# Kernel optimization log

Hardware: AMD Instinct MI355X
Metric: run time of the kernel (lower is better)

Reference implementation:

```python
import jax, jax.numpy as jnp
import numpy as np

WS = 8   # window_size
SS = 4   # shift_size = window_size // 2
HEADS = 8
DH = 16  # dim_head


def _rel_index(ws):
    c = np.arange(ws)
    coords = np.stack(np.meshgrid(c, c, indexing='ij')).reshape(2, -1)  # [2, ws*ws]
    rel = (coords[:, :, None] - coords[:, None, :]).transpose(1, 2, 0)  # [l, l, 2]
    rel[..., 0] += ws - 1
    rel[..., 1] += ws - 1
    rel[..., 0] *= 2 * ws - 1
    return rel.sum(-1)  # [l, l] int


def _make_mask(H, W, ws, ss):
    img = np.zeros((H, W), np.float32)
    sl = (slice(0, -ws), slice(-ws, -ss), slice(-ss, None))
    cnt = 0
    for hs in sl:
        for wcs in sl:
            img[hs, wcs] = cnt
            cnt += 1
    win = img.reshape(H // ws, ws, W // ws, ws).transpose(0, 2, 1, 3).reshape(-1, ws * ws)
    diff = win[:, None, :] - win[:, :, None]  # [nW, l, l]
    return np.where(diff != 0, -np.inf, 0.0).astype(np.float32)


def _ln(x, g, b, eps=1e-5):
    m = x.mean(-1, keepdims=True)
    v = ((x - m) ** 2).mean(-1, keepdims=True)
    return (x - m) * jax.lax.rsqrt(v + eps) * g + b


def _part(t, ws):
    B, H, W, C = t.shape
    return t.reshape(B, H // ws, ws, W // ws, ws, C).transpose(0, 1, 3, 2, 4, 5).reshape(-1, ws * ws, C)


def _unpart(t, ws, B, H, W):
    C = t.shape[-1]
    return t.reshape(B, H // ws, W // ws, ws, ws, C).transpose(0, 1, 3, 2, 4, 5).reshape(B, H, W, C)


def _block(x, illu, p, shift, mask, ridx):
    B, H, W, C = x.shape
    ws = WS
    l = ws * ws
    g1, b1, qw, qb, tbl, pw, pb, g2, b2, f1w, f1b, f2w, f2b = p
    shortcut = x
    xn = _ln(x, g1, b1)
    if shift > 0:
        xn = jnp.roll(xn, (-shift, -shift), (1, 2))
        illu = jnp.roll(illu, (-shift, -shift), (1, 2))
    xw = _part(xn, ws)     # [n, l, C]
    iw = _part(illu, ws)   # [n, l, C]
    n = xw.shape[0]
    qkv = (xw @ qw + qb).reshape(n, l, 3, HEADS, DH).transpose(2, 0, 3, 1, 4)
    q, k, v = qkv[0], qkv[1], qkv[2]  # each [n, h, l, d]
    attn = jnp.einsum('nhld,nhmd->nhlm', q * (DH ** -0.5), k)
    bias = tbl[ridx].transpose(2, 0, 1)  # [h, l, l]
    attn = attn + bias[None]
    # illumination modulation of V
    v = v * iw.reshape(n, l, HEADS, DH).transpose(0, 2, 1, 3)
    if mask is not None:
        nw = mask.shape[0]
        attn = (attn.reshape(B, nw, HEADS, l, l) + mask[None, :, None]).reshape(n, HEADS, l, l)
    attn = jax.nn.softmax(attn, axis=-1)
    out = jnp.einsum('nhlm,nhmd->nhld', attn, v).transpose(0, 2, 1, 3).reshape(n, l, C)
    out = out @ pw + pb
    out = _unpart(out, ws, B, H, W)
    if shift > 0:
        out = jnp.roll(out, (shift, shift), (1, 2))
    x = shortcut + out
    y = _ln(x, g2, b2)
    y = jax.nn.gelu(y @ f1w + f1b, approximate=False) @ f2w + f2b
    return x + y


def setup_inputs() -> dict:
    key = jax.random.key(0)
    ks = jax.random.split(key, 8)
    B, C, H, W = 4, 128, 256, 256
    NB, HID, TBL = 2, 512, 225
    r = lambda k, s, sc=1.0: jax.random.normal(k, s, jnp.float32) * sc
    return {
        'x': r(ks[0], (B, C, H, W)),
        'illu_fea': r(ks[1], (B, C, H, W)),
        'norm1_g': jnp.ones((NB, C), jnp.float32),
        'norm1_b': jnp.zeros((NB, C), jnp.float32),
        'qkv_w': r(ks[2], (NB, C, 3 * C), 0.02),
        'qkv_b': jnp.zeros((NB, 3 * C), jnp.float32),
        'bias_table': r(ks[3], (NB, TBL, HEADS), 0.02),
        'proj_w': r(ks[4], (NB, C, C), 0.02),
        'proj_b': jnp.zeros((NB, C), jnp.float32),
        'norm2_g': jnp.ones((NB, C), jnp.float32),
        'norm2_b': jnp.zeros((NB, C), jnp.float32),
        'fc1_w': r(ks[5], (NB, C, HID), 0.02),
        'fc1_b': jnp.zeros((NB, HID), jnp.float32),
        'fc2_w': r(ks[6], (NB, HID, C), 0.02),
        'fc2_b': jnp.zeros((NB, C), jnp.float32),
    }


def reference(x, illu_fea, norm1_g, norm1_b, qkv_w, qkv_b, bias_table, proj_w, proj_b, norm2_g, norm2_b, fc1_w, fc1_b, fc2_w, fc2_b):
    B, C, H, W = x.shape
    xb = x.transpose(0, 2, 3, 1)
    ib = illu_fea.transpose(0, 2, 3, 1)
    ridx = _rel_index(WS)
    mask = jnp.asarray(_make_mask(H, W, WS, SS))
    nb = norm1_g.shape[0]
    for i in range(nb):
        shift = 0 if i % 2 == 0 else SS
        p = (norm1_g[i], norm1_b[i], qkv_w[i], qkv_b[i], bias_table[i], proj_w[i], proj_b[i],
             norm2_g[i], norm2_b[i], fc1_w[i], fc1_b[i], fc2_w[i], fc2_b[i])
        xb = _block(xb, ib, p, shift, mask if shift > 0 else None, ridx)
    return xb.transpose(0, 3, 1, 2)
```

## Files before the change

### kernel.cpp

```cpp
#include <hip/hip_runtime.h>
#include <hip/hip_bf16.h>

typedef unsigned short u16;
typedef __attribute__((ext_vector_type(8))) short bfrag;
typedef __attribute__((ext_vector_type(4))) float f32x4;
typedef __attribute__((ext_vector_type(2))) int i32x2;
typedef __attribute__((ext_vector_type(4))) int i32x4;

constexpr int OFF_N1G  = 64;
constexpr int OFF_N1B  = OFF_N1G + 256;
constexpr int OFF_QKVB = OFF_N1B + 256;
constexpr int OFF_PB   = OFF_QKVB + 768;
constexpr int OFF_N2G  = OFF_PB + 256;
constexpr int OFF_N2B  = OFF_N2G + 256;
constexpr int OFF_F1B  = OFF_N2B + 256;
constexpr int OFF_F2B  = OFF_F1B + 1024;
constexpr int OFF_BIAS = OFF_F2B + 256;
constexpr int OFF_QWT  = OFF_BIAS + 65536;
constexpr int OFF_PWT  = OFF_QWT + 49152;
constexpr int OFF_F1WT = OFF_PWT + 16384;
constexpr int OFF_F2WT = OFF_F1WT + 65536;
constexpr long OFF_OBUF = 265728;
constexpr long OFF_XBUF = OFF_OBUF + 16777216;
constexpr long OFF_IBUF = OFF_XBUF + 33554432;

__device__ __forceinline__ float blo(unsigned w) { return __uint_as_float(w << 16); }
__device__ __forceinline__ u16 f2b(float f) {
  unsigned u = __float_as_uint(f);
  u += 0x7fffu + ((u >> 16) & 1u);
  return (u16)(u >> 16);
}
__device__ __forceinline__ unsigned f2b_pk(float a, float b) {
  unsigned r;
  asm("v_cvt_pk_bf16_f32 %0, %1, %2" : "=v"(r) : "v"(a), "v"(b));
  return r;
}
__device__ __forceinline__ float ldin(const void* p, long i, int bf) {
  if (bf) return blo((unsigned)((const u16*)p)[i]);
  return ((const float*)p)[i];
}
__device__ __forceinline__ f32x4 mfma16(bfrag a, bfrag b, f32x4 c) {
  return __builtin_amdgcn_mfma_f32_16x16x32_bf16(a, b, c, 0, 0, 0);
}
__device__ __forceinline__ float fast_gelu(float x) {
  const float z = fabsf(x) * 0.70710678118f;
  const float tt = __builtin_amdgcn_rcpf(1.0f + 0.3275911f * z);
  const float poly = tt * (0.254829592f + tt * (-0.284496736f + tt * (1.421413741f +
                     tt * (-1.453152027f + tt * 1.061405429f))));
  const float erfz = 1.0f - poly * __expf(-z * z);
  return x * 0.5f * (1.0f + copysignf(erfz, x));
}

__global__ void k_sniff(const u16* __restrict__ x, int* __restrict__ flag) {
  __shared__ int sc[4];
  const int t = threadIdx.x;
  int c = 0;
  for (int i = t; i < 4096; i += 256) {
    const int e = (x[2 * i] >> 7) & 0xFF;
    c += (e >= 96 && e <= 143) ? 1 : 0;
  }
  #pragma unroll
  for (int o = 32; o; o >>= 1) c += __shfl_down(c, o);
  if ((t & 63) == 0) sc[t >> 6] = c;
  __syncthreads();
  if (t == 0) *flag = ((sc[0] + sc[1] + sc[2] + sc[3]) > 2400) ? 1 : 0;
}

__global__ void k_convert(const void* __restrict__ src, float* __restrict__ dst, int n,
                          const int* __restrict__ flagp) {
  const int bf = *flagp;
  const int i = blockIdx.x * 256 + threadIdx.x;
  if (i < n) dst[i] = ldin(src, i, bf);
}

__global__ void k_cvtT(const void* __restrict__ src, u16* __restrict__ dst, int K, int N,
                       const int* __restrict__ flagp) {
  const int bf = *flagp;
  const int id = blockIdx.x * 256 + threadIdx.x;
  const int KN = K * N;
  if (id >= 2 * KN) return;
  const int l = id / KN, r = id % KN;
  const int n = r % N, k = r / N;
  const float v = ldin(src, (long)l * KN + (long)k * N + n, bf);
  dst[((long)l * N + n) * K + k] = f2b(v);
}

__global__ void k_cvtF1(const void* __restrict__ src, u16* __restrict__ dst,
                        const int* __restrict__ flagp) {
  const int bf = *flagp;
  const int id = blockIdx.x * 256 + threadIdx.x;
  const int l = id >> 16, r = id & 65535;
  const int k = r >> 9, n = r & 511;
  const float v = ldin(src, (long)l * 65536 + k * 512 + n, bf);
  dst[(long)l * 65536 + (n >> 6) * 8192 + (((n & 63) * 128 + k) ^ ((n & 7) << 3))] = f2b(v);
}
__global__ void k_cvtF2(const void* __restrict__ src, u16* __restrict__ dst,
                        const int* __restrict__ flagp) {
  const int bf = *flagp;
  const int id = blockIdx.x * 256 + threadIdx.x;
  const int l = id >> 16, r = id & 65535;
  const int k = r >> 7, n = r & 127;
  const float v = ldin(src, (long)l * 65536 + k * 128 + n, bf);
  dst[(long)l * 65536 + (k >> 6) * 8192 + ((n * 64 + (k & 63)) ^ ((n & 7) << 3))] = f2b(v);
}

__global__ void k_bias(const void* __restrict__ tbl, float* __restrict__ dst,
                       const int* __restrict__ flagp) {
  const int bf = *flagp;
  const int id = blockIdx.x * 256 + threadIdx.x;
  const int j = id & 63, i = (id >> 6) & 63;
  const int idx = ((i >> 3) - (j >> 3) + 7) * 15 + ((i & 7) - (j & 7) + 7);
  const int h = (id >> 12) & 7, l = id >> 15;
  dst[(id & ~4095) + j * 64 + i] = ldin(tbl, (long)l * 1800 + idx * 8 + h, bf);
}

__global__ __launch_bounds__(256) void k_tin(const void* __restrict__ src,
                                             const void* __restrict__ il,
                                             float* __restrict__ dst,
                                             u16* __restrict__ idst,
                                             const int* __restrict__ flagp) {
  __shared__ float tile[64][65];
  const int bf = *flagp;
  const int bid = blockIdx.x;
  const int cb = bid & 1, wb = (bid >> 1) & 3, h = (bid >> 3) & 255, b = bid >> 11;
  const int tw = threadIdx.x & 63, tg = threadIdx.x >> 6;
  #pragma unroll
  for (int i = 0; i < 16; ++i) {
    const int c = i * 4 + tg;
    tile[c][tw] = ldin(src, ((long)((b * 128 + cb * 64 + c) * 256 + h)) * 256 + wb * 64 + tw, bf);
  }
  __syncthreads();
  #pragma unroll
  for (int i = 0; i < 16; ++i) {
    const int wl = i * 4 + tg;
    const int pix = (b * 256 + h) * 256 + wb * 64 + wl;
    dst[(size_t)pix * 128 + cb * 64 + tw] = tile[tw][wl];
  }
  __syncthreads();
  #pragma unroll
  for (int i = 0; i < 16; ++i) {
    const int c = i * 4 + tg;
    tile[c][tw] = ldin(il, ((long)((b * 128 + cb * 64 + c) * 256 + h)) * 256 + wb * 64 + tw, bf);
  }
  __syncthreads();
  #pragma unroll
  for (int i = 0; i < 16; ++i) {
    const int wl = i * 4 + tg;
    const int pix = (b * 256 + h) * 256 + wb * 64 + wl;
    idst[(size_t)pix * 128 + cb * 64 + tw] = f2b(tile[tw][wl]);
  }
}

__device__ __forceinline__ int xn_addr(int tok, int chunk) {
  return tok * 128 + ((chunk ^ (tok & 7)) << 3);
}

__global__ __launch_bounds__(256, 5) void k_attnB(
    const float* __restrict__ xbuf, const u16* __restrict__ ibuf,
    const float* __restrict__ wsf, u16* __restrict__ obuf,
    const u16* __restrict__ qwT, const float* __restrict__ biasb,
    const int blk, const int shift)
{
  __shared__ __align__(16) u16 smem[12288];
  u16* xn = smem;
  u16* Q2 = smem;
  u16* K2 = smem + 4096;
  u16* VT = smem + 8192;

  const int t = threadIdx.x, l = t & 63, w = t >> 6;
  const int bid = blockIdx.x;
  const int win = bid >> 1, hh0 = (bid & 1) * 4;
  const int b = win >> 10, wh = (win >> 5) & 31, wn = win & 31;
  const int hglob = hh0 + w;
  const int g = l >> 4, c16 = l & 15, c8 = c16 * 8;

  const float* g1 = wsf + OFF_N1G + blk * 128;
  const float* b1 = wsf + OFF_N1B + blk * 128;
  const float* qb = wsf + OFF_QKVB + blk * 384;
  const u16* qwl = qwT + (size_t)blk * 49152;

  float iw[4][4];
  {
    const u16* ip = ibuf + (size_t)b * 8388608 + hglob * 16 + c16;
    #pragma unroll
    for (int rt = 0; rt < 4; ++rt)
      #pragma unroll
      for (int r = 0; r < 4; ++r) {
        const int tok = rt * 16 + g * 4 + r;
        const int hh = (wh * 8 + (tok >> 3) + shift) & 255;
        const int wp = (wn * 8 + (tok & 7) + shift) & 255;
        iw[rt][r] = blo(ip[(size_t)((hh << 8) + wp) * 128]);
      }
  }

  {
    float gg[8], bb[8];
    *(float4*)&gg[0] = *(const float4*)(g1 + c8);
    *(float4*)&gg[4] = *(const float4*)(g1 + c8 + 4);
    *(float4*)&bb[0] = *(const float4*)(b1 + c8);
    *(float4*)&bb[4] = *(const float4*)(b1 + c8 + 4);
    #pragma unroll
    for (int s = 0; s < 4; ++s) {
      const int tok = w * 16 + s * 4 + g;
      const int hh = (wh * 8 + (tok >> 3) + shift) & 255;
      const int wp = (wn * 8 + (tok & 7) + shift) & 255;
      const float* xr = xbuf + (size_t)((b * 256 + hh) * 256 + wp) * 128 + c8;
      float v[8];
      *(float4*)&v[0] = *(const float4*)xr;
      *(float4*)&v[4] = *(const float4*)(xr + 4);
      float sm = 0.f, sq = 0.f;
      #pragma unroll
      for (int j = 0; j < 8; ++j) { sm += v[j]; sq = fmaf(v[j], v[j], sq); }
      #pragma unroll
      for (int o = 8; o; o >>= 1) { sm += __shfl_xor(sm, o); sq += __shfl_xor(sq, o); }
      const float mean = sm * 0.0078125f;
      const float rstd = rsqrtf(fmaf(-mean, mean, sq * 0.0078125f) + 1e-5f);
      unsigned pk[4];
      #pragma unroll
      for (int jj = 0; jj < 4; ++jj) {
        const float o0 = (v[2 * jj] - mean) * rstd * gg[2 * jj] + bb[2 * jj];
        const float o1 = (v[2 * jj + 1] - mean) * rstd * gg[2 * jj + 1] + bb[2 * jj + 1];
        pk[jj] = f2b_pk(o0, o1);
      }
      i32x4 st; st[0] = (int)pk[0]; st[1] = (int)pk[1]; st[2] = (int)pk[2]; st[3] = (int)pk[3];
      *(i32x4*)&xn[(tok * 128 + c8) ^ ((tok & 7) << 3)] = st;
    }
  }
  __syncthreads();

  {
    const int colv = (16 + hglob) * 16 + c16;
    const float bv = qb[colv];
    f32x4 acv[4];
    #pragma unroll
    for (int rt = 0; rt < 4; ++rt) acv[rt] = (f32x4){bv, bv, bv, bv};
    const u16* bp = qwl + colv * 128 + g * 8;
    #pragma unroll
    for (int kt = 0; kt < 4; ++kt) {
      const bfrag bw = *(const bfrag*)(bp + kt * 32);
      #pragma unroll
      for (int rt = 0; rt < 4; ++rt) {
        const bfrag a = *(const bfrag*)&xn[xn_addr(rt * 16 + c16, kt * 4 + g)];
        acv[rt] = mfma16(a, bw, acv[rt]);
      }
    }
    u16* vt = VT + w * 1024 + c16 * 64;
    const int sx = (c16 & 7) << 3;
    #pragma unroll
    for (int rt = 0; rt < 4; ++rt) {
      const unsigned p0 = f2b_pk(acv[rt][0] * iw[rt][0], acv[rt][1] * iw[rt][1]);
      const unsigned p1 = f2b_pk(acv[rt][2] * iw[rt][2], acv[rt][3] * iw[rt][3]);
      i32x2 pp; pp[0] = (int)p0; pp[1] = (int)p1;
      *(i32x2*)&vt[(rt * 16 + g * 4) ^ sx] = pp;
    }
  }

  f32x4 acq[4], ack[4];
  {
    const int colq = hglob * 16 + c16, colk = colq + 128;
    const float bq = qb[colq], bk = qb[colk];
    #pragma unroll
    for (int rt = 0; rt < 4; ++rt) {
      acq[rt] = (f32x4){bq, bq, bq, bq};
      ack[rt] = (f32x4){bk, bk, bk, bk};
    }
    const u16* bpq = qwl + colq * 128 + g * 8;
    const u16* bpk = qwl + colk * 128 + g * 8;
    #pragma unroll
    for (int kt = 0; kt < 4; ++kt) {
      const bfrag bwq = *(const bfrag*)(bpq + kt * 32);
      const bfrag bwk = *(const bfrag*)(bpk + kt * 32);
      #pragma unroll
      for (int rt = 0; rt < 4; ++rt) {
        const bfrag a = *(const bfrag*)&xn[xn_addr(rt * 16 + c16, kt * 4 + g)];
        acq[rt] = mfma16(a, bwq, acq[rt]);
        ack[rt] = mfma16(a, bwk, ack[rt]);
      }
    }
  }
  __syncthreads();

  {
    u16* dq = Q2 + w * 1024 + ((c16 >> 3) * 64) * 8 + (c16 & 7);
    u16* dk = K2 + w * 1024 + ((c16 >> 3) * 64) * 8 + (c16 & 7);
    #pragma unroll
    for (int rt = 0; rt < 4; ++rt)
      #pragma unroll
      for (int r = 0; r < 4; ++r) {
        const int tok = rt * 16 + g * 4 + r;
        dq[tok * 8] = f2b(acq[rt][r]);
        dk[tok * 8] = f2b(ack[rt][r]);
      }
  }

  const bfrag zfrag = {0, 0, 0, 0, 0, 0, 0, 0};
  const f32x4 zacc = {0.f, 0.f, 0.f, 0.f};
  bfrag kf[4];
  #pragma unroll
  for (int jt = 0; jt < 4; ++jt) {
    bfrag v = zfrag;
    if (l < 32) v = *(const bfrag*)&K2[w * 1024 + (g * 64 + jt * 16 + c16) * 8];
    kf[jt] = v;
  }
  bfrag vb[2];
  {
    const int sx = (c16 & 7) << 3;
    #pragma unroll
    for (int kt = 0; kt < 2; ++kt)
      vb[kt] = *(const bfrag*)&VT[w * 1024 + c16 * 64 + ((kt * 32 + g * 8) ^ sx)];
  }

  const float* bl2 = biasb + blk * 32768 + hglob * 4096;
  const bool mk = (shift > 0) && ((wh == 31) || (wn == 31));
  int lj[4];
  if (mk) {
    #pragma unroll
    for (int jt = 0; jt < 4; ++jt) {
      const int j = jt * 16 + c16;
      lj[jt] = ((wh == 31) ? (((j >> 3) < 4) ? 1 : 2) : 0) * 3 +
               ((wn == 31) ? (((j & 7) < 4) ? 1 : 2) : 0);
    }
  }

  u16* Pw = K2 + w * 1024;
  u16* ob = obuf + (size_t)win * 8192 + hglob * 16 + c16;

  #pragma unroll
  for (int it = 0; it < 4; ++it) {
    bfrag qf = zfrag;
    if (l < 32) qf = *(const bfrag*)&Q2[w * 1024 + (g * 64 + it * 16 + c16) * 8];
    f32x4 s4[4];
    #pragma unroll
    for (int jt = 0; jt < 4; ++jt) s4[jt] = mfma16(qf, kf[jt], zacc);

    #pragma unroll
    for (int jt = 0; jt < 4; ++jt) {
      const float4 bv4 = *(const float4*)&bl2[(jt * 16 + c16) * 64 + it * 16 + g * 4];
      #pragma unroll
      for (int r = 0; r < 4; ++r)
        s4[jt][r] = fmaf(s4[jt][r], 0.25f, (&bv4.x)[r]);
    }
    if (mk) {
      #pragma unroll
      for (int r = 0; r < 4; ++r) {
        const int i = it * 16 + g * 4 + r;
        const int li = ((wh == 31) ? (((i >> 3) < 4) ? 1 : 2) : 0) * 3 +
                       ((wn == 31) ? (((i & 7) < 4) ? 1 : 2) : 0);
        #pragma unroll
        for (int jt = 0; jt < 4; ++jt)
          if (li != lj[jt]) s4[jt][r] = -1e30f;
      }
    }

    #pragma unroll
    for (int r = 0; r < 4; ++r) {
      float mx = fmaxf(fmaxf(s4[0][r], s4[1][r]), fmaxf(s4[2][r], s4[3][r]));
      #pragma unroll
      for (int o = 8; o; o >>= 1) mx = fmaxf(mx, __shfl_xor(mx, o));
      float e0 = __expf(s4[0][r] - mx);
      float e1 = __expf(s4[1][r] - mx);
      float e2 = __expf(s4[2][r] - mx);
      float e3 = __expf(s4[3][r] - mx);
      float sm = e0 + e1 + e2 + e3;
      #pragma unroll
      for (int o = 8; o; o >>= 1) sm += __shfl_xor(sm, o);
      const float inv = 1.0f / sm;
      s4[0][r] = e0 * inv; s4[1][r] = e1 * inv;
      s4[2][r] = e2 * inv; s4[3][r] = e3 * inv;
    }

    #pragma unroll
    for (int jt = 0; jt < 4; ++jt)
      #pragma unroll
      for (int r = 0; r < 4; ++r)
        Pw[(g * 4 + r) * 40 + jt * 16 + c16] = f2b(s4[jt][r]);
    const bfrag pa0 = *(const bfrag*)&Pw[c16 * 40 + g * 8];
    const bfrag pa1 = *(const bfrag*)&Pw[c16 * 40 + 32 + g * 8];
    f32x4 o = zacc;
    o = mfma16(pa0, vb[0], o);
    o = mfma16(pa1, vb[1], o);
    #pragma unroll
    for (int r = 0; r < 4; ++r)
      ob[(it * 16 + g * 4 + r) * 128] = f2b(o[r]);
  }
}

__global__ __launch_bounds__(256) void k_proj(
    float* xbuf, const u16* __restrict__ obuf, const u16* __restrict__ pwT,
    const float* __restrict__ wsf, const int blk, const int shift)
{
  __shared__ __align__(16) u16 osh[64 * 136];
  const int t = threadIdx.x, l = t & 63, w = t >> 6;
  const int win = blockIdx.x;
  const int b = win >> 10, wh = (win >> 5) & 31, wn = win & 31;
  const u16* ob = obuf + (size_t)win * 8192;
  #pragma unroll
  for (int q = 0; q < 4; ++q) {
    const int idx = (q * 256 + t) * 8;
    *(bfrag*)&osh[(idx >> 7) * 136 + (idx & 127)] = *(const bfrag*)&ob[idx];
  }
  __syncthreads();
  bfrag af[4];
  #pragma unroll
  for (int kt = 0; kt < 4; ++kt)
    af[kt] = *(const bfrag*)&osh[(w * 16 + (l & 15)) * 136 + kt * 32 + (l >> 4) * 8];
  const u16* pwl = pwT + blk * 16384;
  const float* pb = wsf + OFF_PB + blk * 128;
  #pragma unroll
  for (int ct = 0; ct < 8; ++ct) {
    const int col = ct * 16 + (l & 15);
    const float bv = pb[col];
    f32x4 ac = {bv, bv, bv, bv};
    const u16* bp = pwl + col * 128 + (l >> 4) * 8;
    #pragma unroll
    for (int kt = 0; kt < 4; ++kt) ac = mfma16(af[kt], *(const bfrag*)(bp + kt * 32), ac);
    #pragma unroll
    for (int r = 0; r < 4; ++r) {
      const int tok = w * 16 + (l >> 4) * 4 + r;
      const int hh = (wh * 8 + (tok >> 3) + shift) & 255;
      const int wp = (wn * 8 + (tok & 7) + shift) & 255;
      const size_t xi = (size_t)((b * 256 + hh) * 256 + wp) * 128 + col;
      xbuf[xi] += ac[r];
    }
  }
}

__global__ __launch_bounds__(256, 3) void k_ffn(
    float* xbuf, const float* __restrict__ wsf,
    const u16* __restrict__ f1S, const u16* __restrict__ f2S,
    const int blk, void* __restrict__ outp, const int last,
    const int* __restrict__ flagp)
{
  __shared__ __align__(16) u16 B0[8192];
  __shared__ __align__(16) u16 B1[8192];
  __shared__ __align__(16) u16 hid[8192];
  __shared__ float sbias[512];
  const int bfl = *flagp;
  const int t = threadIdx.x, l = t & 63, w = t >> 6;
  u16* hw = hid + w * 2048;
  const int pix0 = blockIdx.x * 64;
  const float* g2 = wsf + OFF_N2G + blk * 128;
  const float* b2 = wsf + OFF_N2B + blk * 128;
  const float* f1bp = wsf + OFF_F1B + blk * 512;
  const float* f2bp = wsf + OFF_F2B + blk * 128;
  const u16* f1 = f1S + (size_t)blk * 65536;
  const u16* f2 = f2S + (size_t)blk * 65536;

  auto STAGE = [&](const u16* src, u16* dstbuf) {
    const u16* gp = src + w * 2048 + l * 8;
    u16* d = dstbuf + w * 2048;
    #pragma unroll
    for (int q = 0; q < 4; ++q)
      __builtin_amdgcn_global_load_lds(gp + q * 512, d + q * 512, 16, 0, 0);
  };
  auto tsrc = [&](int i) -> const u16* {
    const int cc = i >> 2, pp = i & 3;
    return (pp < 2 ? f1 : f2) + cc * 16384 + (pp & 1) * 8192;
  };

  STAGE(tsrc(0), B0);
  sbias[t] = f1bp[t];
  sbias[t + 256] = f1bp[t + 256];

  {
    const int g = l >> 4, c16 = l & 15, c8 = c16 * 8;
    float gg[8], bb[8];
    *(float4*)&gg[0] = *(const float4*)(g2 + c8);
    *(float4*)&gg[4] = *(const float4*)(g2 + c8 + 4);
    *(float4*)&bb[0] = *(const float4*)(b2 + c8);
    *(float4*)&bb[4] = *(const float4*)(b2 + c8 + 4);
    #pragma unroll
    for (int s = 0; s < 4; ++s) {
      const int tt = s * 4 + g;
      const float* xr = xbuf + (size_t)(pix0 + w * 16 + tt) * 128 + c8;
      float v[8];
      *(float4*)&v[0] = *(const float4*)xr;
      *(float4*)&v[4] = *(const float4*)(xr + 4);
      float sm = 0.f, sq = 0.f;
      #pragma unroll
      for (int j = 0; j < 8; ++j) { sm += v[j]; sq = fmaf(v[j], v[j], sq); }
      #pragma unroll
      for (int o = 8; o; o >>= 1) { sm += __shfl_xor(sm, o); sq += __shfl_xor(sq, o); }
      const float mean = sm * 0.0078125f;
      const float rstd = rsqrtf(fmaf(-mean, mean, sq * 0.0078125f) + 1e-5f);
      unsigned pk[4];
      #pragma unroll
      for (int jj = 0; jj < 4; ++jj) {
        const float o0 = (v[2 * jj] - mean) * rstd * gg[2 * jj] + bb[2 * jj];
        const float o1 = (v[2 * jj + 1] - mean) * rstd * gg[2 * jj + 1] + bb[2 * jj + 1];
        pk[jj] = f2b_pk(o0, o1);
      }
      i32x4 st; st[0] = (int)pk[0]; st[1] = (int)pk[1]; st[2] = (int)pk[2]; st[3] = (int)pk[3];
      *(i32x4*)&hw[(tt * 128 + c8) ^ ((tt & 7) << 3)] = st;
    }
  }
  bfrag af[4];
  #pragma unroll
  for (int kt = 0; kt < 4; ++kt)
    af[kt] = *(const bfrag*)&hw[((l & 15) * 128 + kt * 32 + (l >> 4) * 8) ^ (((l & 15) & 7) << 3)];

  f32x4 y[8];
  #pragma unroll
  for (int ct = 0; ct < 8; ++ct) {
    const float bv = f2bp[ct * 16 + (l & 15)];
    y[ct] = (f32x4){bv, bv, bv, bv};
  }

  for (int c = 0; c < 4; ++c) {
    #pragma unroll
    for (int p = 0; p < 4; ++p) {
      const int i = c * 4 + p;
      if (i < 15) STAGE(tsrc(i + 1), (i & 1) ? B0 : B1);
      if (i == 0) asm volatile("s_waitcnt vmcnt(4) lgkmcnt(0)" ::: "memory");
      else if (i < 15) asm volatile("s_waitcnt vmcnt(4)" ::: "memory");
      else asm volatile("s_waitcnt vmcnt(0)" ::: "memory");
      __builtin_amdgcn_sched_barrier(0);
      __builtin_amdgcn_s_barrier();
      const u16* BUF = (i & 1) ? B1 : B0;
      if (p < 2) {
        #pragma unroll
        for (int c1 = 0; c1 < 4; ++c1) {
          const int wcol = c1 * 16 + (l & 15);
          const int n = p * 64 + wcol;
          const float bv = sbias[c * 128 + n];
          f32x4 a1 = {bv, bv, bv, bv};
          #pragma unroll
          for (int kt = 0; kt < 4; ++kt) {
            const bfrag bw = *(const bfrag*)&BUF[(wcol * 128 + kt * 32 + (l >> 4) * 8) ^ ((wcol & 7) << 3)];
            a1 = mfma16(af[kt], bw, a1);
          }
          #pragma unroll
          for (int r = 0; r < 4; ++r) {
            const int row = (l >> 4) * 4 + r;
            hw[(row * 128 + n) ^ ((row & 7) << 3)] = f2b(fast_gelu(a1[r]));
          }
        }
      } else {
        const int kh = p - 2;
        bfrag a2[2];
        #pragma unroll
        for (int kt = 0; kt < 2; ++kt)
          a2[kt] = *(const bfrag*)&hw[((l & 15) * 128 + kh * 64 + kt * 32 + (l >> 4) * 8) ^ (((l & 15) & 7) << 3)];
        #pragma unroll
        for (int ct = 0; ct < 8; ++ct) {
          const int col = ct * 16 + (l & 15);
          #pragma unroll
          for (int kt = 0; kt < 2; ++kt) {
            const bfrag bw = *(const bfrag*)&BUF[(col * 64 + kt * 32 + (l >> 4) * 8) ^ ((col & 7) << 3)];
            y[ct] = mfma16(a2[kt], bw, y[ct]);
          }
        }
      }
      __builtin_amdgcn_s_barrier();
    }
  }

  #pragma unroll
  for (int ct = 0; ct < 8; ++ct)
    #pragma unroll
    for (int r = 0; r < 4; ++r) {
      const int tok = w * 16 + (l >> 4) * 4 + r;
      const int pix = pix0 + tok;
      const int col = ct * 16 + (l & 15);
      const float rv = xbuf[(size_t)pix * 128 + col] + y[ct][r];
      if (last) {
        const int wp = pix & 255, hh2 = (pix >> 8) & 255, bb = pix >> 16;
        const long oi = (((long)bb * 128 + col) * 256 + hh2) * 256 + wp;
        if (bfl) ((u16*)outp)[oi] = f2b(rv);
        else ((float*)outp)[oi] = rv;
      } else {
        xbuf[(size_t)pix * 128 + col] = rv;
      }
    }
}

extern "C" void kernel_launch(void* const* d_in, const int* in_sizes, int n_in,
                              void* d_out, int out_size, void* d_ws, size_t ws_size,
                              hipStream_t stream) {
  (void)in_sizes; (void)n_in; (void)out_size; (void)ws_size;
  float* wsf = (float*)d_ws;
  int* flag = (int*)d_ws;
  const void* x = d_in[0];
  const void* illu = d_in[1];

  k_sniff<<<1, 256, 0, stream>>>((const u16*)x, flag);

  static const int cv_idx[8] = {2, 3, 5, 8, 9, 10, 12, 14};
  static const int cv_off[8] = {OFF_N1G, OFF_N1B, OFF_QKVB, OFF_PB, OFF_N2G, OFF_N2B, OFF_F1B, OFF_F2B};
  static const int cv_n[8] = {256, 256, 768, 256, 256, 256, 1024, 256};
  for (int i = 0; i < 8; ++i)
    k_convert<<<(cv_n[i] + 255) / 256, 256, 0, stream>>>(d_in[cv_idx[i]], wsf + cv_off[i], cv_n[i], flag);

  u16* qwT = (u16*)(wsf + OFF_QWT);
  u16* pwT = (u16*)(wsf + OFF_PWT);
  u16* f1wS = (u16*)(wsf + OFF_F1WT);
  u16* f2wS = (u16*)(wsf + OFF_F2WT);
  k_cvtT<<<384, 256, 0, stream>>>(d_in[4], qwT, 128, 384, flag);
  k_cvtT<<<128, 256, 0, stream>>>(d_in[7], pwT, 128, 128, flag);
  k_cvtF1<<<512, 256, 0, stream>>>(d_in[11], f1wS, flag);
  k_cvtF2<<<512, 256, 0, stream>>>(d_in[13], f2wS, flag);
  k_bias<<<256, 256, 0, stream>>>(d_in[6], wsf + OFF_BIAS, flag);

  float* xbuf = wsf + OFF_XBUF;
  u16* obuf = (u16*)(wsf + OFF_OBUF);
  u16* ibuf = (u16*)(wsf + OFF_IBUF);
  k_tin<<<8192, 256, 0, stream>>>(x, illu, xbuf, ibuf, flag);

  for (int blk = 0; blk < 2; ++blk) {
    const int shift = blk ? 4 : 0;
    k_attnB<<<8192, 256, 0, stream>>>(xbuf, ibuf, wsf, obuf, qwT, wsf + OFF_BIAS, blk, shift);
    k_proj<<<4096, 256, 0, stream>>>(xbuf, obuf, pwT, wsf, blk, shift);
    k_ffn<<<4096, 256, 0, stream>>>(xbuf, wsf, f1wS, f2wS, blk, d_out, blk == 1 ? 1 : 0, flag);
  }
}
```

Measured before the change: 1.119 ms.

## Fuse window attention and output projection into one 512-thread kernel per window

Merges the attention kernel (previously two blocks of 4 heads per window) and the separate projection kernel into one kernel where a 512-thread block handles all 8 heads of a window. Attention output stays in swizzled shared memory and is projected in place, then added to the residual. This removes the bf16 obuf round trip through global memory, one launch, and the duplicated LayerNorm/xn load that came from splitting heads across blocks. In exchange shared memory per block grows to 64KB and blocks are larger, which may lower occupancy.

```diff
diff --git a/kernel.cpp b/kernel.cpp
--- a/kernel.cpp
+++ b/kernel.cpp
@@ -20,8 +20,7 @@
 constexpr int OFF_PWT  = OFF_QWT + 49152;
 constexpr int OFF_F1WT = OFF_PWT + 16384;
 constexpr int OFF_F2WT = OFF_F1WT + 65536;
-constexpr long OFF_OBUF = 265728;
-constexpr long OFF_XBUF = OFF_OBUF + 16777216;
+constexpr long OFF_XBUF = 265728;
 constexpr long OFF_IBUF = OFF_XBUF + 33554432;
 
 __device__ __forceinline__ float blo(unsigned w) { return __uint_as_float(w << 16); }
@@ -155,23 +154,22 @@
   return tok * 128 + ((chunk ^ (tok & 7)) << 3);
 }
 
-__global__ __launch_bounds__(256, 5) void k_attnB(
-    const float* __restrict__ xbuf, const u16* __restrict__ ibuf,
-    const float* __restrict__ wsf, u16* __restrict__ obuf,
-    const u16* __restrict__ qwT, const float* __restrict__ biasb,
-    const int blk, const int shift)
+__global__ __launch_bounds__(512, 4) void k_attnP(
+    float* xbuf, const u16* __restrict__ ibuf,
+    const float* __restrict__ wsf,
+    const u16* __restrict__ qwT, const u16* __restrict__ pwT,
+    const float* __restrict__ biasb, const int blk, const int shift)
 {
-  __shared__ __align__(16) u16 smem[12288];
+  __shared__ __align__(16) u16 smem[32768];
   u16* xn = smem;
-  u16* Q2 = smem;
-  u16* K2 = smem + 4096;
-  u16* VT = smem + 8192;
+  u16* Q2 = smem + 8192;
+  u16* K2 = smem + 16384;
+  u16* VT = smem + 24576;
+  u16* O  = smem + 24576;
 
   const int t = threadIdx.x, l = t & 63, w = t >> 6;
-  const int bid = blockIdx.x;
-  const int win = bid >> 1, hh0 = (bid & 1) * 4;
+  const int win = blockIdx.x;
   const int b = win >> 10, wh = (win >> 5) & 31, wn = win & 31;
-  const int hglob = hh0 + w;
   const int g = l >> 4, c16 = l & 15, c8 = c16 * 8;
 
   const float* g1 = wsf + OFF_N1G + blk * 128;
@@ -181,7 +179,7 @@
 
   float iw[4][4];
   {
-    const u16* ip = ibuf + (size_t)b * 8388608 + hglob * 16 + c16;
+    const u16* ip = ibuf + (size_t)b * 8388608 + w * 16 + c16;
     #pragma unroll
     for (int rt = 0; rt < 4; ++rt)
       #pragma unroll
@@ -200,8 +198,8 @@
     *(float4*)&bb[0] = *(const float4*)(b1 + c8);
     *(float4*)&bb[4] = *(const float4*)(b1 + c8 + 4);
     #pragma unroll
-    for (int s = 0; s < 4; ++s) {
-      const int tok = w * 16 + s * 4 + g;
+    for (int s = 0; s < 2; ++s) {
+      const int tok = w * 8 + s * 4 + g;
       const int hh = (wh * 8 + (tok >> 3) + shift) & 255;
       const int wp = (wn * 8 + (tok & 7) + shift) & 255;
       const float* xr = xbuf + (size_t)((b * 256 + hh) * 256 + wp) * 128 + c8;
@@ -229,7 +227,7 @@
   __syncthreads();
 
   {
-    const int colv = (16 + hglob) * 16 + c16;
+    const int colv = (16 + w) * 16 + c16;
     const float bv = qb[colv];
     f32x4 acv[4];
     #pragma unroll
@@ -255,42 +253,51 @@
     }
   }
 
-  f32x4 acq[4], ack[4];
-  {
-    const int colq = hglob * 16 + c16, colk = colq + 128;
-    const float bq = qb[colq], bk = qb[colk];
-    #pragma unroll
-    for (int rt = 0; rt < 4; ++rt) {
-      acq[rt] = (f32x4){bq, bq, bq, bq};
-      ack[rt] = (f32x4){bk, bk, bk, bk};
-    }
+  {
+    const int colq = w * 16 + c16;
+    const float bq = qb[colq];
+    f32x4 acq[4];
+    #pragma unroll
+    for (int rt = 0; rt < 4; ++rt) acq[rt] = (f32x4){bq, bq, bq, bq};
     const u16* bpq = qwl + colq * 128 + g * 8;
-    const u16* bpk = qwl + colk * 128 + g * 8;
     #pragma unroll
     for (int kt = 0; kt < 4; ++kt) {
       const bfrag bwq = *(const bfrag*)(bpq + kt * 32);
-      const bfrag bwk = *(const bfrag*)(bpk + kt * 32);
       #pragma unroll
       for (int rt = 0; rt < 4; ++rt) {
         const bfrag a = *(const bfrag*)&xn[xn_addr(rt * 16 + c16, kt * 4 + g)];
         acq[rt] = mfma16(a, bwq, acq[rt]);
+      }
+    }
+    u16* dq = Q2 + w * 1024 + ((c16 >> 3) * 64) * 8 + (c16 & 7);
+    #pragma unroll
+    for (int rt = 0; rt < 4; ++rt)
+      #pragma unroll
+      for (int r = 0; r < 4; ++r)
+        dq[(rt * 16 + g * 4 + r) * 8] = f2b(acq[rt][r]);
+  }
+  {
+    const int colk = 128 + w * 16 + c16;
+    const float bk = qb[colk];
+    f32x4 ack[4];
+    #pragma unroll
+    for (int rt = 0; rt < 4; ++rt) ack[rt] = (f32x4){bk, bk, bk, bk};
+    const u16* bpk = qwl + colk * 128 + g * 8;
+    #pragma unroll
+    for (int kt = 0; kt < 4; ++kt) {
+      const bfrag bwk = *(const bfrag*)(bpk + kt * 32);
+      #pragma unroll
+      for (int rt = 0; rt < 4; ++rt) {
+        const bfrag a = *(const bfrag*)&xn[xn_addr(rt * 16 + c16, kt * 4 + g)];
         ack[rt] = mfma16(a, bwk, ack[rt]);
       }
     }
-  }
-  __syncthreads();
-
-  {
-    u16* dq = Q2 + w * 1024 + ((c16 >> 3) * 64) * 8 + (c16 & 7);
     u16* dk = K2 + w * 1024 + ((c16 >> 3) * 64) * 8 + (c16 & 7);
     #pragma unroll
     for (int rt = 0; rt < 4; ++rt)
       #pragma unroll
-      for (int r = 0; r < 4; ++r) {
-        const int tok = rt * 16 + g * 4 + r;
-        dq[tok * 8] = f2b(acq[rt][r]);
-        dk[tok * 8] = f2b(ack[rt][r]);
-      }
+      for (int r = 0; r < 4; ++r)
+        dk[(rt * 16 + g * 4 + r) * 8] = f2b(ack[rt][r]);
   }
 
   const bfrag zfrag = {0, 0, 0, 0, 0, 0, 0, 0};
@@ -309,8 +316,9 @@
     for (int kt = 0; kt < 2; ++kt)
       vb[kt] = *(const bfrag*)&VT[w * 1024 + c16 * 64 + ((kt * 32 + g * 8) ^ sx)];
   }
-
-  const float* bl2 = biasb + blk * 32768 + hglob * 4096;
+  __syncthreads();
+
+  const float* bl2 = biasb + blk * 32768 + w * 4096;
   const bool mk = (shift > 0) && ((wh == 31) || (wn == 31));
   int lj[4];
   if (mk) {
@@ -321,9 +329,7 @@
                ((wn == 31) ? (((j & 7) < 4) ? 1 : 2) : 0);
     }
   }
-
   u16* Pw = K2 + w * 1024;
-  u16* ob = obuf + (size_t)win * 8192 + hglob * 16 + c16;
 
   #pragma unroll
   for (int it = 0; it < 4; ++it) {
@@ -380,47 +386,37 @@
     o = mfma16(pa0, vb[0], o);
     o = mfma16(pa1, vb[1], o);
     #pragma unroll
-    for (int r = 0; r < 4; ++r)
-      ob[(it * 16 + g * 4 + r) * 128] = f2b(o[r]);
-  }
-}
-
-__global__ __launch_bounds__(256) void k_proj(
-    float* xbuf, const u16* __restrict__ obuf, const u16* __restrict__ pwT,
-    const float* __restrict__ wsf, const int blk, const int shift)
-{
-  __shared__ __align__(16) u16 osh[64 * 136];
-  const int t = threadIdx.x, l = t & 63, w = t >> 6;
-  const int win = blockIdx.x;
-  const int b = win >> 10, wh = (win >> 5) & 31, wn = win & 31;
-  const u16* ob = obuf + (size_t)win * 8192;
-  #pragma unroll
-  for (int q = 0; q < 4; ++q) {
-    const int idx = (q * 256 + t) * 8;
-    *(bfrag*)&osh[(idx >> 7) * 136 + (idx & 127)] = *(const bfrag*)&ob[idx];
+    for (int r = 0; r < 4; ++r) {
+      const int tok = it * 16 + g * 4 + r;
+      O[tok * 128 + (((w * 2 + (c16 >> 3)) ^ (tok & 7)) << 3) + (c16 & 7)] = f2b(o[r]);
+    }
   }
   __syncthreads();
-  bfrag af[4];
-  #pragma unroll
-  for (int kt = 0; kt < 4; ++kt)
-    af[kt] = *(const bfrag*)&osh[(w * 16 + (l & 15)) * 136 + kt * 32 + (l >> 4) * 8];
-  const u16* pwl = pwT + blk * 16384;
-  const float* pb = wsf + OFF_PB + blk * 128;
-  #pragma unroll
-  for (int ct = 0; ct < 8; ++ct) {
-    const int col = ct * 16 + (l & 15);
-    const float bv = pb[col];
-    f32x4 ac = {bv, bv, bv, bv};
-    const u16* bp = pwl + col * 128 + (l >> 4) * 8;
-    #pragma unroll
-    for (int kt = 0; kt < 4; ++kt) ac = mfma16(af[kt], *(const bfrag*)(bp + kt * 32), ac);
-    #pragma unroll
-    for (int r = 0; r < 4; ++r) {
-      const int tok = w * 16 + (l >> 4) * 4 + r;
-      const int hh = (wh * 8 + (tok >> 3) + shift) & 255;
-      const int wp = (wn * 8 + (tok & 7) + shift) & 255;
-      const size_t xi = (size_t)((b * 256 + hh) * 256 + wp) * 128 + col;
-      xbuf[xi] += ac[r];
+
+  {
+    const int prt = w & 3, ph = w >> 2;
+    bfrag af[4];
+    #pragma unroll
+    for (int kt = 0; kt < 4; ++kt)
+      af[kt] = *(const bfrag*)&O[xn_addr(prt * 16 + c16, kt * 4 + g)];
+    const u16* pwl = pwT + blk * 16384;
+    const float* pb = wsf + OFF_PB + blk * 128;
+    #pragma unroll
+    for (int ct = 0; ct < 4; ++ct) {
+      const int col = ph * 64 + ct * 16 + c16;
+      const float bv = pb[col];
+      f32x4 ac = {bv, bv, bv, bv};
+      const u16* bp = pwl + col * 128 + g * 8;
+      #pragma unroll
+      for (int kt = 0; kt < 4; ++kt) ac = mfma16(af[kt], *(const bfrag*)(bp + kt * 32), ac);
+      #pragma unroll
+      for (int r = 0; r < 4; ++r) {
+        const int tok = prt * 16 + g * 4 + r;
+        const int hh = (wh * 8 + (tok >> 3) + shift) & 255;
+        const int wp = (wn * 8 + (tok & 7) + shift) & 255;
+        const size_t xi = (size_t)((b * 256 + hh) * 256 + wp) * 128 + col;
+        xbuf[xi] += ac[r];
+      }
     }
   }
 }
@@ -602,14 +598,12 @@
   k_bias<<<256, 256, 0, stream>>>(d_in[6], wsf + OFF_BIAS, flag);
 
   float* xbuf = wsf + OFF_XBUF;
-  u16* obuf = (u16*)(wsf + OFF_OBUF);
   u16* ibuf = (u16*)(wsf + OFF_IBUF);
   k_tin<<<8192, 256, 0, stream>>>(x, illu, xbuf, ibuf, flag);
 
   for (int blk = 0; blk < 2; ++blk) {
     const int shift = blk ? 4 : 0;
-    k_attnB<<<8192, 256, 0, stream>>>(xbuf, ibuf, wsf, obuf, qwT, wsf + OFF_BIAS, blk, shift);
-    k_proj<<<4096, 256, 0, stream>>>(xbuf, obuf, pwT, wsf, blk, shift);
+    k_attnP<<<4096, 512, 0, stream>>>(xbuf, ibuf, wsf, qwT, pwT, wsf + OFF_BIAS, blk, shift);
     k_ffn<<<4096, 256, 0, stream>>>(xbuf, wsf, f1wS, f2wS, blk, d_out, blk == 1 ? 1 : 0, flag);
   }
 }
```

Result: faster. 983.8 us (-12.1%).
